# Kernel tuning notes

Measured on AMD Instinct MI355X. Metric: run time of the kernel, lower is better.

## Reference

```python
import jax, jax.numpy as jnp
import numpy as np

B, D, H, W = 2, 64, 128, 128
LARGE = 1e8  # sentinel squared distance (no surface found yet)


def setup_inputs() -> dict:
    key = jax.random.key(0)
    k1, k2 = jax.random.split(key)
    pred = jax.random.normal(k1, (B, 1, D, H, W), dtype=jnp.float32)
    # binary ground-truth mask stored as float, as in the torch module
    target = jax.random.randint(k2, (B, 1, D, H, W), 0, 2).astype(jnp.float32)
    return {"pred": pred, "target": target}


def _erode(m):
    """scipy.ndimage.binary_erosion with default 6-connectivity structure,
    border_value=0 (out-of-bounds treated as background)."""
    e = m
    for ax in range(3):
        pad = [(1, 1) if i == ax else (0, 0) for i in range(3)]
        p = jnp.pad(m, pad)  # False padding
        n = m.shape[ax]
        lo = jax.lax.slice_in_dim(p, 0, n, axis=ax)      # m[i-1]
        hi = jax.lax.slice_in_dim(p, 2, n + 2, axis=ax)  # m[i+1]
        e = e & lo & hi
    return e


def _edt_pass(d2, axis):
    """One separable pass of the exact squared EDT:
    out[i] = min_j (d2[j] + (i-j)^2) along `axis` (Felzenszwalb decomposition,
    computed by brute-force broadcast min, vectorized over all lines)."""
    moved = jnp.moveaxis(d2, axis, 0)
    moved_shape = moved.shape
    n = moved_shape[0]
    x = moved.reshape(n, -1)  # (n, rest)
    idx = jnp.arange(n, dtype=d2.dtype)
    diff2 = (idx[:, None] - idx[None, :]) ** 2  # (n_out, n_in)
    out = jnp.min(x[None, :, :] + diff2[:, :, None], axis=1)  # (n_out, rest)
    return jnp.moveaxis(out.reshape(moved_shape), 0, axis)


def _surface_distance(mask):
    """Distance from every voxel to the nearest surface voxel, where
    surface = mask & ~binary_erosion(mask). Matches
    ndimage.distance_transform_edt(~surface) (exact Euclidean)."""
    eroded = _erode(mask)
    surface = mask & ~eroded
    d2 = jnp.where(surface, jnp.float32(0.0), jnp.float32(LARGE))
    for ax in range(3):
        d2 = _edt_pass(d2, ax)
    return jnp.sqrt(d2)


def _smooth_l1(a, b):
    d = a - b
    ad = jnp.abs(d)
    return jnp.mean(jnp.where(ad < 1.0, 0.5 * d * d, ad - 0.5))


def reference(pred, target):
    p = jax.nn.sigmoid(pred)
    pred_mask = p[:, 0] > 0.5       # (B, D, H, W) bool
    target_mask = target[:, 0] != 0  # astype(bool)

    def per_sample(pm, tm):
        return _smooth_l1(_surface_distance(pm), _surface_distance(tm))

    losses = jax.vmap(per_sample)(pred_mask, target_mask)  # (B,)
    return jnp.mean(losses)
```

## Files before the change

kernel.cpp:

```cpp
#include <hip/hip_runtime.h>

#define D_ 64
#define H_ 128
#define W_ 128
#define VOL (D_*H_*W_)
#define NF 4
#define LARGEF 1e8f
#define SW(r,c) (((r) << 7) + ((c) ^ ((r) & 31)))

__device__ __forceinline__ bool maskv(float v, int which) {
  return which ? (v != 0.0f) : (v > 0.0f);
}

__global__ __launch_bounds__(256) void k_init(const float* __restrict__ pred,
                                              const float* __restrict__ targ,
                                              unsigned char* __restrict__ surf,
                                              double* __restrict__ acc) {
  int idx = blockIdx.x * 256 + threadIdx.x;
  if (idx < 3) acc[idx] = 0.0;
  int f = idx >> 18;
  int q = idx & 262143;
  int which = f & 1;
  const float* __restrict__ src = (which ? targ : pred) + ((size_t)(f >> 1) << 20);
  const float4* __restrict__ s4 = (const float4*)src;
  int v = q << 2;
  int z = v >> 14, y = (v >> 7) & 127, x = v & 127;
  float4 c = s4[q];
  bool m0 = maskv(c.x, which), m1 = maskv(c.y, which);
  bool m2 = maskv(c.z, which), m3 = maskv(c.w, which);
  bool ym0=false, ym1=false, ym2=false, ym3=false;
  bool yp0=false, yp1=false, yp2=false, yp3=false;
  bool zm0=false, zm1=false, zm2=false, zm3=false;
  bool zp0=false, zp1=false, zp2=false, zp3=false;
  if (y > 0)   { float4 t = s4[q - 32];   ym0=maskv(t.x,which); ym1=maskv(t.y,which); ym2=maskv(t.z,which); ym3=maskv(t.w,which); }
  if (y < 127) { float4 t = s4[q + 32];   yp0=maskv(t.x,which); yp1=maskv(t.y,which); yp2=maskv(t.z,which); yp3=maskv(t.w,which); }
  if (z > 0)   { float4 t = s4[q - 4096]; zm0=maskv(t.x,which); zm1=maskv(t.y,which); zm2=maskv(t.z,which); zm3=maskv(t.w,which); }
  if (z < 63)  { float4 t = s4[q + 4096]; zp0=maskv(t.x,which); zp1=maskv(t.y,which); zp2=maskv(t.z,which); zp3=maskv(t.w,which); }
  bool lm = (x > 0)   ? maskv(src[v - 1], which) : false;
  bool rm = (x < 124) ? maskv(src[v + 4], which) : false;
  bool e0 = m0 && lm && m1 && ym0 && yp0 && zm0 && zp0;
  bool e1 = m1 && m0 && m2 && ym1 && yp1 && zm1 && zp1;
  bool e2 = m2 && m1 && m3 && ym2 && yp2 && zm2 && zp2;
  bool e3 = m3 && m2 && rm && ym3 && yp3 && zm3 && zp3;
  uchar4 o;
  o.x = (unsigned char)(m0 && !e0);
  o.y = (unsigned char)(m1 && !e1);
  o.z = (unsigned char)(m2 && !e2);
  o.w = (unsigned char)(m3 && !e3);
  ((uchar4*)surf)[idx] = o;
}

__global__ __launch_bounds__(256) void k_zscan(const unsigned char* __restrict__ surf,
                                               unsigned char* __restrict__ zdist) {
  __shared__ unsigned short fwd[D_][256];
  int g = blockIdx.x * 256 + threadIdx.x;
  int f = g >> 14, yx = g & 16383;
  const unsigned char* s = surf + (f << 20) + yx;
  unsigned char* o = zdist + (f << 20) + yx;
  int d = 255;
  #pragma unroll 16
  for (int z = 0; z < D_; ++z) {
    d = s[z << 14] ? 0 : min(d + 1, 255);
    fwd[z][threadIdx.x] = (unsigned short)d;
  }
  int dd = 255;
  #pragma unroll 8
  for (int z = D_ - 1; z >= 0; --z) {
    int fv = fwd[z][threadIdx.x];
    dd = (fv == 0) ? 0 : min(dd + 1, 255);
    o[z << 14] = (unsigned char)min(fv, dd);
  }
}

__global__ __launch_bounds__(1024) void k_edt_yx(const unsigned char* __restrict__ zdist,
                                                 float* __restrict__ dist) {
  __shared__ float tile[128 * 128];
  int f = blockIdx.y, z = blockIdx.x;
  const uchar4* __restrict__ z4 = (const uchar4*)(zdist + (f << 20) + (z << 14));
  float* dbase = dist + (f << 20) + (z << 14);
  #pragma unroll
  for (int e4 = threadIdx.x, i = 0; i < 4; ++i, e4 += 1024) {
    int r = e4 >> 5, c0 = (e4 & 31) << 2;
    uchar4 bb = z4[e4];
    float r2 = (float)(r * r);
    tile[SW(r, c0 + 0)] = ((bb.x == 255) ? LARGEF : (float)(bb.x * bb.x)) + r2;
    tile[SW(r, c0 + 1)] = ((bb.y == 255) ? LARGEF : (float)(bb.y * bb.y)) + r2;
    tile[SW(r, c0 + 2)] = ((bb.z == 255) ? LARGEF : (float)(bb.z * bb.z)) + r2;
    tile[SW(r, c0 + 3)] = ((bb.w == 255) ? LARGEF : (float)(bb.w * bb.w)) + r2;
  }
  __syncthreads();
  const int R = 16;
  int tp = threadIdx.x & 127, tw = threadIdx.x >> 7;
  float best[R], fi[R];
  float fb = (float)(tw * R);
  float tmax = 0.0f;
  #pragma unroll
  for (int u = 0; u < R; ++u) {
    fi[u] = fb + (float)u; best[u] = 3.0e8f;
    float tv = tile[SW(tw * R + u, tp)] - fi[u] * fi[u];
    tmax = fmaxf(tmax, tv);
  }
  #pragma unroll
  for (int o = 1; o < 64; o <<= 1) tmax = fmaxf(tmax, __shfl_xor(tmax, o));
  int rad = (int)sqrtf(tmax);
  int jlo = max(0, tw * R - rad), jhi = min(H_ - 1, tw * R + (R - 1) + rad);
  for (int j = jlo; j <= jhi; ++j) {
    float t = tile[SW(j, tp)];
    float m2j = -2.0f * (float)j;
    #pragma unroll
    for (int u = 0; u < R; ++u)
      best[u] = fminf(best[u], __builtin_fmaf(m2j, fi[u], t));
  }
  __syncthreads();
  float fx2 = (float)(tp * tp);
  #pragma unroll
  for (int u = 0; u < R; ++u)
    tile[SW(tw * R + u, tp)] = best[u] + fi[u] * fi[u] + fx2;
  __syncthreads();
  tmax = 0.0f;
  #pragma unroll
  for (int u = 0; u < R; ++u) {
    best[u] = 3.0e8f;
    float tv = tile[SW(tp, tw * R + u)] - fi[u] * fi[u];
    tmax = fmaxf(tmax, tv);
  }
  #pragma unroll
  for (int o = 1; o < 64; o <<= 1) tmax = fmaxf(tmax, __shfl_xor(tmax, o));
  rad = (int)sqrtf(tmax);
  jlo = max(0, tw * R - rad); jhi = min(W_ - 1, tw * R + (R - 1) + rad);
  for (int j = jlo; j <= jhi; ++j) {
    float t = tile[SW(tp, j)];
    float m2j = -2.0f * (float)j;
    #pragma unroll
    for (int u = 0; u < R; ++u)
      best[u] = fminf(best[u], __builtin_fmaf(m2j, fi[u], t));
  }
  __syncthreads();
  #pragma unroll
  for (int u = 0; u < R; ++u)
    tile[SW(tp, tw * R + u)] = sqrtf(best[u] + fi[u] * fi[u]);
  __syncthreads();
  for (int e = threadIdx.x; e < 16384; e += 1024)
    dbase[e] = tile[SW(e >> 7, e & 127)];
}

__global__ __launch_bounds__(256) void k_reduce(const float* __restrict__ dist,
                                               double* __restrict__ acc,
                                               float* __restrict__ out) {
  int b = blockIdx.y;
  const float4* dp = (const float4*)(dist + ((size_t)(b * 2 + 0) << 20));
  const float4* dt = (const float4*)(dist + ((size_t)(b * 2 + 1) << 20));
  double s = 0.0;
  for (int v = blockIdx.x * 256 + threadIdx.x; v < VOL / 4; v += gridDim.x * 256) {
    float4 a = dp[v], c = dt[v];
    float d0 = a.x - c.x, d1 = a.y - c.y, d2v = a.z - c.z, d3 = a.w - c.w;
    float a0 = fabsf(d0), a1 = fabsf(d1), a2 = fabsf(d2v), a3 = fabsf(d3);
    s += (double)(a0 < 1.0f ? 0.5f * d0 * d0 : a0 - 0.5f);
    s += (double)(a1 < 1.0f ? 0.5f * d1 * d1 : a1 - 0.5f);
    s += (double)(a2 < 1.0f ? 0.5f * d2v * d2v : a2 - 0.5f);
    s += (double)(a3 < 1.0f ? 0.5f * d3 * d3 : a3 - 0.5f);
  }
  for (int o = 32; o > 0; o >>= 1) s += __shfl_down(s, o);
  __shared__ double wsum[4];
  if ((threadIdx.x & 63) == 0) wsum[threadIdx.x >> 6] = s;
  __syncthreads();
  if (threadIdx.x == 0) {
    atomicAdd(&acc[b], wsum[0] + wsum[1] + wsum[2] + wsum[3]);
    __threadfence();
    unsigned* ctr = (unsigned*)&acc[2];
    unsigned done = atomicAdd(ctr, 1u);
    if (done == gridDim.x * gridDim.y - 1) {
      __threadfence();
      out[0] = (float)(0.5 * (acc[0] / (double)VOL + acc[1] / (double)VOL));
    }
  }
}

extern "C" void kernel_launch(void* const* d_in, const int* in_sizes, int n_in,
                              void* d_out, int out_size, void* d_ws, size_t ws_size,
                              hipStream_t stream) {
  const float* pred = (const float*)d_in[0];
  const float* targ = (const float*)d_in[1];
  unsigned char* surf  = (unsigned char*)d_ws;
  unsigned char* zdist = (unsigned char*)d_ws + ((size_t)NF << 20);
  float*  dist = (float*)((char*)d_ws + ((size_t)NF << 21));
  double* acc  = (double*)((char*)d_ws + ((size_t)NF << 21) + ((size_t)NF * VOL * 4));
  float*  out  = (float*)d_out;

  k_init  <<<NF * VOL / 4 / 256, 256, 0, stream>>>(pred, targ, surf, acc);
  k_zscan <<<NF * H_ * W_ / 256, 256, 0, stream>>>(surf, zdist);
  k_edt_yx<<<dim3(D_, NF), 1024, 0, stream>>>(zdist, dist);
  k_reduce<<<dim3(256, 2), 256, 0, stream>>>(dist, acc, out);
}
```

Baseline: 118.7 us.

## Store squared distances as packed uint16 and defer sqrt to reduce kernel

The EDT kernel now writes squared distances as 16-bit integers directly from registers, skipping the shared-memory transpose and the second store pass. This halves the intermediate buffer that the reduction reads. The reduction unpacks each value, maps the saturated code back to the large sentinel, and takes the sqrt there. The tile load loop now reads bytes instead of uchar4, so it does more load instructions. Exactness relies on every squared distance below the cap being an integer that fits in 16 bits.

```diff
diff --git a/kernel.cpp b/kernel.cpp
--- a/kernel.cpp
+++ b/kernel.cpp
@@ -73,20 +73,15 @@
 }
 
 __global__ __launch_bounds__(1024) void k_edt_yx(const unsigned char* __restrict__ zdist,
-                                                 float* __restrict__ dist) {
+                                                 unsigned short* __restrict__ d2s) {
   __shared__ float tile[128 * 128];
   int f = blockIdx.y, z = blockIdx.x;
-  const uchar4* __restrict__ z4 = (const uchar4*)(zdist + (f << 20) + (z << 14));
-  float* dbase = dist + (f << 20) + (z << 14);
-  #pragma unroll
-  for (int e4 = threadIdx.x, i = 0; i < 4; ++i, e4 += 1024) {
-    int r = e4 >> 5, c0 = (e4 & 31) << 2;
-    uchar4 bb = z4[e4];
-    float r2 = (float)(r * r);
-    tile[SW(r, c0 + 0)] = ((bb.x == 255) ? LARGEF : (float)(bb.x * bb.x)) + r2;
-    tile[SW(r, c0 + 1)] = ((bb.y == 255) ? LARGEF : (float)(bb.y * bb.y)) + r2;
-    tile[SW(r, c0 + 2)] = ((bb.z == 255) ? LARGEF : (float)(bb.z * bb.z)) + r2;
-    tile[SW(r, c0 + 3)] = ((bb.w == 255) ? LARGEF : (float)(bb.w * bb.w)) + r2;
+  const unsigned char* zsrc = zdist + (f << 20) + (z << 14);
+  for (int e = threadIdx.x; e < 16384; e += 1024) {
+    int r = e >> 7, c = e & 127;
+    int b = zsrc[e];
+    float v = (b == 255) ? LARGEF : (float)(b * b);
+    tile[SW(r, c)] = v + (float)(r * r);
   }
   __syncthreads();
   const int R = 16;
@@ -135,30 +130,44 @@
     for (int u = 0; u < R; ++u)
       best[u] = fminf(best[u], __builtin_fmaf(m2j, fi[u], t));
   }
-  __syncthreads();
-  #pragma unroll
-  for (int u = 0; u < R; ++u)
-    tile[SW(tp, tw * R + u)] = sqrtf(best[u] + fi[u] * fi[u]);
-  __syncthreads();
-  for (int e = threadIdx.x; e < 16384; e += 1024)
-    dbase[e] = tile[SW(e >> 7, e & 127)];
-}
-
-__global__ __launch_bounds__(256) void k_reduce(const float* __restrict__ dist,
+  unsigned pk[8];
+  #pragma unroll
+  for (int p = 0; p < 8; ++p) {
+    float dlo = best[2*p]     + fi[2*p]     * fi[2*p];
+    float dhi = best[2*p + 1] + fi[2*p + 1] * fi[2*p + 1];
+    unsigned lo = (dlo > 65504.f) ? 65535u : (unsigned)dlo;
+    unsigned hi = (dhi > 65504.f) ? 65535u : (unsigned)dhi;
+    pk[p] = lo | (hi << 16);
+  }
+  uint4* ob = (uint4*)(d2s + (f << 20) + (z << 14) + (tp << 7) + tw * R);
+  ob[0] = make_uint4(pk[0], pk[1], pk[2], pk[3]);
+  ob[1] = make_uint4(pk[4], pk[5], pk[6], pk[7]);
+}
+
+__global__ __launch_bounds__(256) void k_reduce(const unsigned short* __restrict__ d2s,
                                                double* __restrict__ acc,
                                                float* __restrict__ out) {
   int b = blockIdx.y;
-  const float4* dp = (const float4*)(dist + ((size_t)(b * 2 + 0) << 20));
-  const float4* dt = (const float4*)(dist + ((size_t)(b * 2 + 1) << 20));
+  const uint4* dp = (const uint4*)(d2s + ((size_t)(b * 2 + 0) << 20));
+  const uint4* dt = (const uint4*)(d2s + ((size_t)(b * 2 + 1) << 20));
   double s = 0.0;
-  for (int v = blockIdx.x * 256 + threadIdx.x; v < VOL / 4; v += gridDim.x * 256) {
-    float4 a = dp[v], c = dt[v];
-    float d0 = a.x - c.x, d1 = a.y - c.y, d2v = a.z - c.z, d3 = a.w - c.w;
-    float a0 = fabsf(d0), a1 = fabsf(d1), a2 = fabsf(d2v), a3 = fabsf(d3);
-    s += (double)(a0 < 1.0f ? 0.5f * d0 * d0 : a0 - 0.5f);
-    s += (double)(a1 < 1.0f ? 0.5f * d1 * d1 : a1 - 0.5f);
-    s += (double)(a2 < 1.0f ? 0.5f * d2v * d2v : a2 - 0.5f);
-    s += (double)(a3 < 1.0f ? 0.5f * d3 * d3 : a3 - 0.5f);
+  for (int v = blockIdx.x * 256 + threadIdx.x; v < VOL / 8; v += gridDim.x * 256) {
+    uint4 A = dp[v], C = dt[v];
+    unsigned aw[4] = {A.x, A.y, A.z, A.w};
+    unsigned cw[4] = {C.x, C.y, C.z, C.w};
+    #pragma unroll
+    for (int k = 0; k < 4; ++k) {
+      unsigned a0 = aw[k] & 0xFFFFu, a1 = aw[k] >> 16;
+      unsigned c0 = cw[k] & 0xFFFFu, c1 = cw[k] >> 16;
+      float da0 = sqrtf(a0 == 65535u ? LARGEF : (float)a0);
+      float da1 = sqrtf(a1 == 65535u ? LARGEF : (float)a1);
+      float dc0 = sqrtf(c0 == 65535u ? LARGEF : (float)c0);
+      float dc1 = sqrtf(c1 == 65535u ? LARGEF : (float)c1);
+      float d0 = da0 - dc0, d1 = da1 - dc1;
+      float b0 = fabsf(d0), b1 = fabsf(d1);
+      s += (double)(b0 < 1.0f ? 0.5f * d0 * d0 : b0 - 0.5f);
+      s += (double)(b1 < 1.0f ? 0.5f * d1 * d1 : b1 - 0.5f);
+    }
   }
   for (int o = 32; o > 0; o >>= 1) s += __shfl_down(s, o);
   __shared__ double wsum[4];
@@ -181,14 +190,14 @@
                               hipStream_t stream) {
   const float* pred = (const float*)d_in[0];
   const float* targ = (const float*)d_in[1];
-  unsigned char* surf  = (unsigned char*)d_ws;
-  unsigned char* zdist = (unsigned char*)d_ws + ((size_t)NF << 20);
-  float*  dist = (float*)((char*)d_ws + ((size_t)NF << 21));
-  double* acc  = (double*)((char*)d_ws + ((size_t)NF << 21) + ((size_t)NF * VOL * 4));
-  float*  out  = (float*)d_out;
+  unsigned char*  surf  = (unsigned char*)d_ws;
+  unsigned char*  zdist = (unsigned char*)d_ws + ((size_t)NF << 20);
+  unsigned short* d2s   = (unsigned short*)((char*)d_ws + ((size_t)NF << 21));
+  double* acc = (double*)((char*)d_ws + ((size_t)NF << 21) + ((size_t)NF * VOL * 2));
+  float*  out = (float*)d_out;
 
   k_init  <<<NF * VOL / 4 / 256, 256, 0, stream>>>(pred, targ, surf, acc);
   k_zscan <<<NF * H_ * W_ / 256, 256, 0, stream>>>(surf, zdist);
-  k_edt_yx<<<dim3(D_, NF), 1024, 0, stream>>>(zdist, dist);
-  k_reduce<<<dim3(256, 2), 256, 0, stream>>>(dist, acc, out);
-}
+  k_edt_yx<<<dim3(D_, NF), 1024, 0, stream>>>(zdist, d2s);
+  k_reduce<<<dim3(256, 2), 256, 0, stream>>>(d2s, acc, out);
+}
```

Result: faster. 115.5 us (-2.7%).
